# Optimization experiments

Measured on AMD Instinct MI355X. Metric: run time of the kernel, lower is better.

## Reference

```python
import jax, jax.numpy as jnp
import numpy as np

B, A, NC = 2_000_000, 3, 3  # batch, anchors per sample, num classes


def setup_inputs() -> dict:
    key = jax.random.key(0)
    k1, k2, k3, k4 = jax.random.split(key, 4)
    # output: probabilities in (0,1) since BCELoss expects probs (sigmoid already applied upstream)
    output = jax.random.uniform(k1, (B, A, 1 + 3 + NC), dtype=jnp.float32,
                                minval=1e-4, maxval=1.0 - 1e-4)
    # target: [obj in {0,1} | 3 coords | class index as float]
    obj = jax.random.bernoulli(k2, 0.5, (B, A)).astype(jnp.float32)
    coords = jax.random.uniform(k3, (B, A, 3), dtype=jnp.float32)
    cls = jax.random.randint(k4, (B, A), 0, NC).astype(jnp.float32)
    target = jnp.concatenate([obj[..., None], coords, cls[..., None]], axis=-1)
    return {"output": output, "target": target}


def _bce_sum(p, t):
    # matches torch.nn.BCELoss(reduction='sum'), which clamps log terms at -100
    logp = jnp.maximum(jnp.log(p), -100.0)
    log1mp = jnp.maximum(jnp.log1p(-p), -100.0)
    return -jnp.sum(t * logp + (1.0 - t) * log1mp)


def reference(output, target):
    obj_col = target[:, :, 0]
    target_object = (obj_col == 1.0).astype(output.dtype)
    # one-hot class target (vectorized replacement of the Python scatter loop)
    cls_idx = jax.lax.stop_gradient(target[:, :, -1]).astype(jnp.int32)
    target_classe = jax.nn.one_hot(cls_idx, NC, dtype=output.dtype)  # [B, A, NC]

    xywh_loss = jnp.sum((output[:, :, 1:4] - target[:, :, 1:4]) ** 2)
    class_loss = _bce_sum(output[:, :, 4:], target_classe)
    object_loss = _bce_sum(output[:, :, 0], target_object)
    # note: the original also computes noObjectLoss but never uses it
    return 2.0 * class_loss + 4.0 * xywh_loss + object_loss
```

## Files before the change

### kernel.cpp

```cpp
#include <hip/hip_runtime.h>


#define NROWS  6000000
#define NGROUP (NROWS / 4)
#define LN2F   0.69314718055994530942f

__global__ void init_ws_kernel(double* ws) {
    if (threadIdx.x == 0 && blockIdx.x == 0) ws[0] = 0.0;
}

__global__ __launch_bounds__(256) void det_loss_kernel(
        const float* __restrict__ out,
        const float* __restrict__ tgt,
        double* __restrict__ ws) {
    double acc = 0.0;
    const int nthreads = gridDim.x * blockDim.x;
    for (long long g = (long long)blockIdx.x * blockDim.x + threadIdx.x;
         g < NGROUP; g += nthreads) {
        const float4* po = reinterpret_cast<const float4*>(out + (size_t)g * 28);
        const float4* pt = reinterpret_cast<const float4*>(tgt + (size_t)g * 20);
        float o[28];
        float t[20];
        #pragma unroll
        for (int k = 0; k < 7; ++k) {
            float4 v = po[k];
            o[4*k+0] = v.x; o[4*k+1] = v.y; o[4*k+2] = v.z; o[4*k+3] = v.w;
        }
        #pragma unroll
        for (int k = 0; k < 5; ++k) {
            float4 v = pt[k];
            t[4*k+0] = v.x; t[4*k+1] = v.y; t[4*k+2] = v.z; t[4*k+3] = v.w;
        }
        float xywh = 0.0f;
        float cls_log2 = 0.0f;
        float obj_prod = 1.0f;
        #pragma unroll
        for (int r = 0; r < 4; ++r) {
            const float* orow = o + 7*r;
            const float* trow = t + 5*r;
            float dx = orow[1] - trow[1];
            float dy = orow[2] - trow[2];
            float dz = orow[3] - trow[3];
            xywh += dx*dx + dy*dy + dz*dz;
            int ci = (int)trow[4];
            float c0 = orow[4], c1 = orow[5], c2 = orow[6];
            float f0 = (ci == 0) ? c0 : 1.0f - c0;
            float f1 = (ci == 1) ? c1 : 1.0f - c1;
            float f2 = (ci == 2) ? c2 : 1.0f - c2;
            cls_log2 += __log2f(f0 * f1 * f2);
            float p0 = orow[0];
            obj_prod *= (trow[0] == 1.0f) ? p0 : 1.0f - p0;
        }
        float obj_log2 = __log2f(obj_prod);
        acc += (double)(4.0f * xywh - LN2F * (2.0f * cls_log2 + obj_log2));
    }
    #pragma unroll
    for (int off = 32; off > 0; off >>= 1)
        acc += __shfl_down(acc, off, 64);
    __shared__ double wave_sums[4];
    const int lane = threadIdx.x & 63;
    const int wid  = threadIdx.x >> 6;
    if (lane == 0) wave_sums[wid] = acc;
    __syncthreads();
    if (threadIdx.x == 0) {
        double b = wave_sums[0] + wave_sums[1] + wave_sums[2] + wave_sums[3];
        atomicAdd(ws, b);
    }
}

__global__ void finalize_kernel(const double* ws, float* out) {
    if (threadIdx.x == 0 && blockIdx.x == 0) out[0] = (float)ws[0];
}

extern "C" void kernel_launch(void* const* d_in, const int* in_sizes, int n_in,
                              void* d_out, int out_size, void* d_ws, size_t ws_size,
                              hipStream_t stream) {
    const float* out_p = (const float*)d_in[0];
    const float* tgt_p = (const float*)d_in[1];
    float* res = (float*)d_out;
    double* ws = (double*)d_ws;

    init_ws_kernel<<<1, 64, 0, stream>>>(ws);
    det_loss_kernel<<<2048, 256, 0, stream>>>(out_p, tgt_p, ws);
    finalize_kernel<<<1, 64, 0, stream>>>(ws, res);
}
```

Measured before the change: 304.7 us.

## Stage rows through LDS via direct global-to-LDS loads and drop atomics

Each wave now loads a 64-row quantum of output and target with coalesced dword global_load_lds instructions into per-wave LDS buffers, then each lane reads its own row from LDS. This replaces the per-thread strided float4 loads. The three log calls per row are folded into a single log2 of a combined product. The atomic accumulation and separate init kernel are replaced by per-block partial sums and a single-block final reduction, removing one launch. Risks are that the load-then-wait pattern per iteration has no prefetch overlap, and that multiplying the probabilities before taking the log can underflow.

```diff
diff --git a/kernel.cpp b/kernel.cpp
--- a/kernel.cpp
+++ b/kernel.cpp
@@ -1,75 +1,92 @@
 #include <hip/hip_runtime.h>
 
 
-#define NROWS  6000000
-#define NGROUP (NROWS / 4)
-#define LN2F   0.69314718055994530942f
+#define NROWS   6000000
+#define NQUANTA (NROWS / 64)
+#define GRID    2048
+#define BLOCK   256
+#define NWAVES  (GRID * (BLOCK / 64))
+#define LN2     0.69314718055994530942
 
-__global__ void init_ws_kernel(double* ws) {
-    if (threadIdx.x == 0 && blockIdx.x == 0) ws[0] = 0.0;
-}
+#define GLOAD_LDS(g, l) __builtin_amdgcn_global_load_lds(                     \
+    (const __attribute__((address_space(1))) unsigned int*)(g),               \
+    (__attribute__((address_space(3))) unsigned int*)(l), 4, 0, 0)
 
 __global__ __launch_bounds__(256) void det_loss_kernel(
         const float* __restrict__ out,
         const float* __restrict__ tgt,
-        double* __restrict__ ws) {
-    double acc = 0.0;
-    const int nthreads = gridDim.x * blockDim.x;
-    for (long long g = (long long)blockIdx.x * blockDim.x + threadIdx.x;
-         g < NGROUP; g += nthreads) {
-        const float4* po = reinterpret_cast<const float4*>(out + (size_t)g * 28);
-        const float4* pt = reinterpret_cast<const float4*>(tgt + (size_t)g * 20);
-        float o[28];
-        float t[20];
+        double* __restrict__ partial) {
+    __shared__ float lds_out[4][448];
+    __shared__ float lds_tgt[4][320];
+
+    const int lane  = threadIdx.x & 63;
+    const int wid   = threadIdx.x >> 6;
+    const int gwave = blockIdx.x * 4 + wid;
+
+    float* lo = lds_out[wid];
+    float* lt = lds_tgt[wid];
+
+    float xywh_sum = 0.0f;
+    float log2_sum = 0.0f;
+
+    for (int q = gwave; q < NQUANTA; q += NWAVES) {
+        asm volatile("s_waitcnt lgkmcnt(0)" ::: "memory");
+        const float* po = out + (size_t)q * 448 + lane;
+        const float* pt = tgt + (size_t)q * 320 + lane;
         #pragma unroll
-        for (int k = 0; k < 7; ++k) {
-            float4 v = po[k];
-            o[4*k+0] = v.x; o[4*k+1] = v.y; o[4*k+2] = v.z; o[4*k+3] = v.w;
-        }
+        for (int k = 0; k < 7; ++k)
+            GLOAD_LDS(po + k * 64, lo + k * 64);
         #pragma unroll
-        for (int k = 0; k < 5; ++k) {
-            float4 v = pt[k];
-            t[4*k+0] = v.x; t[4*k+1] = v.y; t[4*k+2] = v.z; t[4*k+3] = v.w;
-        }
-        float xywh = 0.0f;
-        float cls_log2 = 0.0f;
-        float obj_prod = 1.0f;
-        #pragma unroll
-        for (int r = 0; r < 4; ++r) {
-            const float* orow = o + 7*r;
-            const float* trow = t + 5*r;
-            float dx = orow[1] - trow[1];
-            float dy = orow[2] - trow[2];
-            float dz = orow[3] - trow[3];
-            xywh += dx*dx + dy*dy + dz*dz;
-            int ci = (int)trow[4];
-            float c0 = orow[4], c1 = orow[5], c2 = orow[6];
-            float f0 = (ci == 0) ? c0 : 1.0f - c0;
-            float f1 = (ci == 1) ? c1 : 1.0f - c1;
-            float f2 = (ci == 2) ? c2 : 1.0f - c2;
-            cls_log2 += __log2f(f0 * f1 * f2);
-            float p0 = orow[0];
-            obj_prod *= (trow[0] == 1.0f) ? p0 : 1.0f - p0;
-        }
-        float obj_log2 = __log2f(obj_prod);
-        acc += (double)(4.0f * xywh - LN2F * (2.0f * cls_log2 + obj_log2));
+        for (int k = 0; k < 5; ++k)
+            GLOAD_LDS(pt + k * 64, lt + k * 64);
+        asm volatile("s_waitcnt vmcnt(0)" ::: "memory");
+
+        const int b7 = lane * 7;
+        const int b5 = lane * 5;
+        float o0 = lo[b7 + 0], o1 = lo[b7 + 1], o2 = lo[b7 + 2], o3 = lo[b7 + 3];
+        float o4 = lo[b7 + 4], o5 = lo[b7 + 5], o6 = lo[b7 + 6];
+        float t0 = lt[b5 + 0], t1 = lt[b5 + 1], t2 = lt[b5 + 2], t3 = lt[b5 + 3];
+        float t4 = lt[b5 + 4];
+
+        float dx = o1 - t1, dy = o2 - t2, dz = o3 - t3;
+        xywh_sum += dx * dx + dy * dy + dz * dz;
+
+        int ci = (int)t4;
+        float f0 = (ci == 0) ? o4 : 1.0f - o4;
+        float f1 = (ci == 1) ? o5 : 1.0f - o5;
+        float f2 = (ci == 2) ? o6 : 1.0f - o6;
+        float fo = (t0 == 1.0f) ? o0 : 1.0f - o0;
+        float m  = f0 * f1 * f2;
+        float v  = m * m * fo;
+        log2_sum += __log2f(v);
     }
+
+    double val = 4.0 * (double)xywh_sum - LN2 * (double)log2_sum;
     #pragma unroll
     for (int off = 32; off > 0; off >>= 1)
-        acc += __shfl_down(acc, off, 64);
-    __shared__ double wave_sums[4];
+        val += __shfl_down(val, off, 64);
+
+    __shared__ double wsum[4];
+    if (lane == 0) wsum[wid] = val;
+    __syncthreads();
+    if (threadIdx.x == 0)
+        partial[blockIdx.x] = wsum[0] + wsum[1] + wsum[2] + wsum[3];
+}
+
+__global__ __launch_bounds__(256) void final_reduce(
+        const double* __restrict__ partial, float* __restrict__ outp) {
+    double s = 0.0;
+    for (int i = threadIdx.x; i < GRID; i += BLOCK) s += partial[i];
+    #pragma unroll
+    for (int off = 32; off > 0; off >>= 1)
+        s += __shfl_down(s, off, 64);
+    __shared__ double wsum[4];
     const int lane = threadIdx.x & 63;
     const int wid  = threadIdx.x >> 6;
-    if (lane == 0) wave_sums[wid] = acc;
+    if (lane == 0) wsum[wid] = s;
     __syncthreads();
-    if (threadIdx.x == 0) {
-        double b = wave_sums[0] + wave_sums[1] + wave_sums[2] + wave_sums[3];
-        atomicAdd(ws, b);
-    }
-}
-
-__global__ void finalize_kernel(const double* ws, float* out) {
-    if (threadIdx.x == 0 && blockIdx.x == 0) out[0] = (float)ws[0];
+    if (threadIdx.x == 0)
+        outp[0] = (float)(wsum[0] + wsum[1] + wsum[2] + wsum[3]);
 }
 
 extern "C" void kernel_launch(void* const* d_in, const int* in_sizes, int n_in,
@@ -80,7 +97,6 @@
     float* res = (float*)d_out;
     double* ws = (double*)d_ws;
 
-    init_ws_kernel<<<1, 64, 0, stream>>>(ws);
-    det_loss_kernel<<<2048, 256, 0, stream>>>(out_p, tgt_p, ws);
-    finalize_kernel<<<1, 64, 0, stream>>>(ws, res);
+    det_loss_kernel<<<GRID, BLOCK, 0, stream>>>(out_p, tgt_p, ws);
+    final_reduce<<<1, BLOCK, 0, stream>>>(ws, res);
 }
```

Result: no change. 309.0 us (+1.4%).
